# Kernel optimization log

Measured on AMD Instinct MI355X. Metric: run time of the kernel, lower is better.

Reference implementation:

```python
import jax, jax.numpy as jnp
import numpy as np

EPS = 1e-5
H = 8
N_BUCKETS = 32


def _instance_norm(x, gamma, beta):
    # x: [B, N, D]; torch InstanceNorm1d normalizes over the N (length) dim
    # per channel per batch element, using biased variance.
    m = jnp.mean(x, axis=1, keepdims=True)
    v = jnp.var(x, axis=1, keepdims=True)
    return (x - m) * jax.lax.rsqrt(v + EPS) * gamma + beta


def setup_inputs() -> dict:
    key = jax.random.key(0)
    ks = jax.random.split(key, 12)
    B, N, D, d_ff = 4, 512, 128, 512
    s = 1.0 / np.sqrt(D)
    sf = 1.0 / np.sqrt(d_ff)
    u = lambda k, shape, lim: jax.random.uniform(k, shape, jnp.float32, -lim, lim)
    return {
        "h": jax.random.normal(ks[0], (B, N, D), jnp.float32),
        "coords": jax.random.uniform(ks[1], (B, N, 2), jnp.float32),
        "W_Q": u(ks[2], (D, D), s),
        "W_K": u(ks[3], (D, D), s),
        "W_V": u(ks[4], (D, D), s),
        "W_O": u(ks[5], (D, D), s),
        "emb": jax.random.normal(ks[6], (N_BUCKETS, D), jnp.float32),  # n_heads*d_k == D
        "ffn_w1": u(ks[7], (D, d_ff), s),
        "ffn_b1": u(ks[8], (d_ff,), s),
        "ffn_w2": u(ks[9], (d_ff, D), sf),
        "ffn_b2": u(ks[10], (D,), sf),
        "gamma1": jnp.ones((D,), jnp.float32),
        "beta1": jnp.zeros((D,), jnp.float32),
        "gamma2": jnp.ones((D,), jnp.float32),
        "beta2": jnp.zeros((D,), jnp.float32),
    }


def reference(h, coords, W_Q, W_K, W_V, W_O, emb, ffn_w1, ffn_b1, ffn_w2,
              ffn_b2, gamma1, beta1, gamma2, beta2):
    B, N, D = h.shape
    Dk = D // H
    Q = (h @ W_Q).reshape(B, N, H, Dk)
    K = (h @ W_K).reshape(B, N, H, Dk)
    V = (h @ W_V).reshape(B, N, H, Dk)
    # content scores: [B, H, N, N]
    scores = jnp.einsum('bnhd,bmhd->bhnm', Q, K) / np.sqrt(Dk)
    # relative-distance bucket embeddings for all (i, j) pairs
    diff = coords[:, :, None, :] - coords[:, None, :, :]          # [B,N,N,2]
    dist = jax.lax.stop_gradient(jnp.sqrt(jnp.sum(diff * diff, -1)))
    buckets = jnp.clip((dist * N_BUCKETS).astype(jnp.int32), 0, N_BUCKETS - 1)
    r = emb[buckets].reshape(B, N, N, H, Dk)                      # [B,N,N,H,Dk]
    scores = scores + jnp.einsum('bnhd,bnmhd->bhnm', Q, r)
    attn = jax.nn.softmax(scores, axis=-1)
    h_attn = jnp.einsum('bhnm,bmhd->bnhd', attn, V).reshape(B, N, D) @ W_O
    h1 = _instance_norm(h + h_attn, gamma1, beta1)
    h_ffn = jax.nn.relu(h1 @ ffn_w1 + ffn_b1) @ ffn_w2 + ffn_b2
    return _instance_norm(h1 + h_ffn, gamma2, beta2)
```

## Files before the change

kernel.cpp:

```cpp
#include <hip/hip_runtime.h>
#include <hip/hip_bf16.h>

#define B_  4
#define N_  512
#define D_  128
#define H_  8
#define DK  16
#define DFF 512
#define NB  32
#define KS  8

__global__ __launch_bounds__(256) void qkv_qe_kernel(
    const float* __restrict__ A,
    const float* __restrict__ WQ, const float* __restrict__ WK, const float* __restrict__ WV,
    const float* __restrict__ emb,
    float* __restrict__ Qo, float* __restrict__ Ko, float* __restrict__ Vo,
    float* __restrict__ QE)
{
    const float* Bw = blockIdx.z == 0 ? WQ : (blockIdx.z == 1 ? WK : WV);
    float*       C  = blockIdx.z == 0 ? Qo : (blockIdx.z == 1 ? Ko : Vo);
    const int wave = threadIdx.x >> 6;
    const int lane = threadIdx.x & 63;
    const int rbase = __builtin_amdgcn_readfirstlane((blockIdx.x * 4 + wave) * 2);
    const int col = lane * 2;

    float acc[2][2] = {};
#pragma unroll 2
    for (int k0 = 0; k0 < D_; k0 += 4) {
        float4 a0 = *(const float4*)&A[(size_t)(rbase + 0) * D_ + k0];
        float4 a1 = *(const float4*)&A[(size_t)(rbase + 1) * D_ + k0];
#pragma unroll
        for (int kk = 0; kk < 4; ++kk) {
            float2 bv = *(const float2*)&Bw[(size_t)(k0 + kk) * D_ + col];
            float x0 = (&a0.x)[kk], x1 = (&a1.x)[kk];
            acc[0][0] += x0 * bv.x; acc[0][1] += x0 * bv.y;
            acc[1][0] += x1 * bv.x; acc[1][1] += x1 * bv.y;
        }
    }
    *(float2*)&C[(size_t)(rbase + 0) * D_ + col] = make_float2(acc[0][0], acc[0][1]);
    *(float2*)&C[(size_t)(rbase + 1) * D_ + col] = make_float2(acc[1][0], acc[1][1]);

    if (blockIdx.z == 0) {
        __shared__ float Qls[8][132];
        *(float2*)&Qls[wave * 2 + 0][col] = make_float2(acc[0][0], acc[0][1]);
        *(float2*)&Qls[wave * 2 + 1][col] = make_float2(acc[1][0], acc[1][1]);
        __syncthreads();
        const int r  = threadIdx.x >> 5;
        const int hh = (threadIdx.x >> 2) & 7;
        const int k0 = (threadIdx.x & 3) * 8;
        const int grow = blockIdx.x * 8 + r;
        const float4* qv = (const float4*)&Qls[r][hh * DK];
        const float4 qa = qv[0], qb = qv[1], qc = qv[2], qd = qv[3];
        float* qe_out = QE + ((size_t)grow * H_ + hh) * NB + k0;
#pragma unroll 2
        for (int k = 0; k < 8; ++k) {
            const float4* ep = (const float4*)(emb + (size_t)(k0 + k) * D_ + hh * DK);
            float4 e0 = ep[0], e1 = ep[1], e2 = ep[2], e3 = ep[3];
            float d0 = fmaf(qa.x,e0.x, fmaf(qa.y,e0.y, fmaf(qa.z,e0.z, qa.w*e0.w)));
            float d1 = fmaf(qb.x,e1.x, fmaf(qb.y,e1.y, fmaf(qb.z,e1.z, qb.w*e1.w)));
            float d2 = fmaf(qc.x,e2.x, fmaf(qc.y,e2.y, fmaf(qc.z,e2.z, qc.w*e2.w)));
            float d3 = fmaf(qd.x,e3.x, fmaf(qd.y,e3.y, fmaf(qd.z,e3.z, qd.w*e3.w)));
            qe_out[k] = (d0 + d1) + (d2 + d3);
        }
    }
}

__global__ __launch_bounds__(256) void attn6_kernel(
    const float* __restrict__ Q, const float* __restrict__ K, const float* __restrict__ V,
    const float* __restrict__ QE, const float* __restrict__ coords,
    float* __restrict__ P)
{
    const int tid  = threadIdx.x;
    const int wave = tid >> 6;
    const int lane = tid & 63;
    const int bid  = blockIdx.x;
    const int ks    = bid & 7;
    const int chunk = (bid >> 3) & 7;
    const int h     = (bid >> 6) & (H_ - 1);
    const int b     = bid >> 9;
    const int row = b * N_ + chunk * 64 + lane;

    __shared__ float kl[64][16];
    __shared__ float vl[64][16];
    __shared__ float qel[64][NB + 1];
    __shared__ float ckrd[64][2];
    __shared__ float accl[4][64][17];

    const size_t hdbase = (size_t)b * N_ * D_ + h * DK;
    {
        int key = tid >> 2, part = tid & 3;
        size_t g = hdbase + (size_t)(ks * 64 + key) * D_ + part * 4;
        *(float4*)&kl[key][part * 4] = *(const float4*)&K[g];
        *(float4*)&vl[key][part * 4] = *(const float4*)&V[g];
    }
    {
        int r = tid >> 2, part = tid & 3;
        const float* src = QE + ((size_t)(b * N_ + chunk * 64 + r) * H_ + h) * NB + part * 8;
#pragma unroll
        for (int j = 0; j < 8; ++j) qel[r][part * 8 + j] = src[j];
    }
    if (tid < 128)
        ((float*)ckrd)[tid] = coords[(size_t)(b * N_ + ks * 64) * 2 + tid];

    const float4* qp = (const float4*)(Q + (size_t)row * D_ + h * DK);
    const float4 q0 = qp[0], q1 = qp[1], q2 = qp[2], q3 = qp[3];
    const float cx = coords[(size_t)row * 2 + 0];
    const float cy = coords[(size_t)row * 2 + 1];

    __syncthreads();

    float l = 0.f;
    float acc[16] = {};
    const int ml0 = wave * 16;
#pragma unroll 4
    for (int i = 0; i < 16; ++i) {
        const int ml = ml0 + i;
        float dx = cx - ckrd[ml][0], dy = cy - ckrd[ml][1];
        float dist = sqrtf(fmaf(dx, dx, dy * dy));
        int bucket = (int)(dist * 32.0f);
        bucket = bucket > (NB - 1) ? (NB - 1) : bucket;
        float qe = qel[lane][bucket];
        const float4* kp = (const float4*)&kl[ml][0];
        const float4 k0 = kp[0], k1 = kp[1], k2 = kp[2], k3 = kp[3];
        float d0 = fmaf(q0.x,k0.x, fmaf(q0.y,k0.y, fmaf(q0.z,k0.z, q0.w*k0.w)));
        float d1 = fmaf(q1.x,k1.x, fmaf(q1.y,k1.y, fmaf(q1.z,k1.z, q1.w*k1.w)));
        float d2 = fmaf(q2.x,k2.x, fmaf(q2.y,k2.y, fmaf(q2.z,k2.z, q2.w*k2.w)));
        float d3 = fmaf(q3.x,k3.x, fmaf(q3.y,k3.y, fmaf(q3.z,k3.z, q3.w*k3.w)));
        float p = __expf(fmaf((d0 + d1) + (d2 + d3), 0.25f, qe));
        l += p;
        const float4* vp = (const float4*)&vl[ml][0];
        const float4 v0 = vp[0], v1 = vp[1], v2 = vp[2], v3 = vp[3];
        acc[0]  += p * v0.x; acc[1]  += p * v0.y; acc[2]  += p * v0.z; acc[3]  += p * v0.w;
        acc[4]  += p * v1.x; acc[5]  += p * v1.y; acc[6]  += p * v1.z; acc[7]  += p * v1.w;
        acc[8]  += p * v2.x; acc[9]  += p * v2.y; acc[10] += p * v2.z; acc[11] += p * v2.w;
        acc[12] += p * v3.x; acc[13] += p * v3.y; acc[14] += p * v3.z; acc[15] += p * v3.w;
    }

    accl[wave][lane][16] = l;
#pragma unroll
    for (int j = 0; j < 16; ++j) accl[wave][lane][j] = acc[j];
    __syncthreads();

    float* pb = P + (size_t)bid * (64 * 17);
    for (int i = tid; i < 64 * 17; i += 256) {
        int r = i / 17, j = i - r * 17;
        pb[i] = accl[0][r][j] + accl[1][r][j] + accl[2][r][j] + accl[3][r][j];
    }
}

__global__ __launch_bounds__(256) void oproj_kernel(
    const float* __restrict__ P, const float* __restrict__ WO,
    const float* __restrict__ hres, float* __restrict__ X1)
{
    const int tid = threadIdx.x;
    const int gr0 = blockIdx.x * 8;
    __shared__ float AOls[8][128];
    __shared__ float lsl[8][8];

    if (tid < 64) {
        int r = tid >> 3, hh = tid & 7;
        int gr = gr0 + r;
        int b = gr >> 9, n = gr & (N_ - 1);
        int chunk = n >> 6, rl = n & 63;
        size_t base = ((size_t)(((b * H_ + hh) * 8 + chunk) * KS)) * (64 * 17) + (size_t)rl * 17;
        float l = 0.f;
#pragma unroll
        for (int s = 0; s < KS; ++s) l += P[base + (size_t)s * (64 * 17) + 16];
        lsl[r][hh] = l;
    }
    float asum[4];
#pragma unroll
    for (int j = 0; j < 4; ++j) {
        int i = tid + j * 256;
        int r = i >> 7, d = i & 127;
        int gr = gr0 + r;
        int b = gr >> 9, n = gr & (N_ - 1);
        int chunk = n >> 6, rl = n & 63;
        int hh = d >> 4, dk = d & 15;
        size_t base = ((size_t)(((b * H_ + hh) * 8 + chunk) * KS)) * (64 * 17) + (size_t)rl * 17 + dk;
        float s = 0.f;
#pragma unroll
        for (int ss = 0; ss < KS; ++ss) s += P[base + (size_t)ss * (64 * 17)];
        asum[j] = s;
    }
    __syncthreads();
#pragma unroll
    for (int j = 0; j < 4; ++j) {
        int i = tid + j * 256;
        int r = i >> 7, d = i & 127;
        AOls[r][d] = asum[j] / lsl[r][d >> 4];
    }
    __syncthreads();

    const int wave = tid >> 6;
    const int lane = tid & 63;
    const int rl = wave * 2;
    const int grb = __builtin_amdgcn_readfirstlane(gr0 + rl);
    const int col = lane * 2;

    float acc[2][2] = {};
#pragma unroll 2
    for (int k0 = 0; k0 < D_; k0 += 4) {
        float4 a0 = *(const float4*)&AOls[rl + 0][k0];
        float4 a1 = *(const float4*)&AOls[rl + 1][k0];
#pragma unroll
        for (int kk = 0; kk < 4; ++kk) {
            float2 bv = *(const float2*)&WO[(size_t)(k0 + kk) * D_ + col];
            float x0 = (&a0.x)[kk], x1 = (&a1.x)[kk];
            acc[0][0] += x0 * bv.x; acc[0][1] += x0 * bv.y;
            acc[1][0] += x1 * bv.x; acc[1][1] += x1 * bv.y;
        }
    }
#pragma unroll
    for (int j = 0; j < 2; ++j) {
        float2 rv = *(const float2*)&hres[(size_t)(grb + j) * D_ + col];
        *(float2*)&X1[(size_t)(grb + j) * D_ + col] =
            make_float2(acc[j][0] + rv.x, acc[j][1] + rv.y);
    }
}

__global__ __launch_bounds__(256) void stats_kernel(const float* __restrict__ X,
    const float* __restrict__ gamma, const float* __restrict__ beta,
    float* __restrict__ T1, float* __restrict__ T2)
{
    const int b  = blockIdx.x >> 5;
    const int dg = blockIdx.x & 31;
    const int dl = threadIdx.x & 3;
    const int nc = threadIdx.x >> 2;
    const float* xp = X + ((size_t)b * N_ + nc * 8) * D_ + dg * 4 + dl;
    float s = 0.f, q = 0.f;
#pragma unroll
    for (int i = 0; i < 8; ++i) { float x = xp[(size_t)i * D_]; s += x; q += x * x; }
    __shared__ float rs[64][4], rq[64][4];
    rs[nc][dl] = s; rq[nc][dl] = q;
    __syncthreads();
    for (int off = 32; off >= 1; off >>= 1) {
        if (nc < off) { rs[nc][dl] += rs[nc + off][dl]; rq[nc][dl] += rq[nc + off][dl]; }
        __syncthreads();
    }
    if (threadIdx.x < 4) {
        int d = dg * 4 + threadIdx.x;
        float mean = rs[0][threadIdx.x] * (1.0f / N_);
        float var  = rq[0][threadIdx.x] * (1.0f / N_) - mean * mean;
        float r = 1.0f / sqrtf(var + 1e-5f);
        float t1 = r * gamma[d];
        T1[b * D_ + d] = t1;
        T2[b * D_ + d] = beta[d] - mean * t1;
    }
}

__global__ __launch_bounds__(256) void ffn1_kernel(
    const float* __restrict__ X1, const float* __restrict__ T1, const float* __restrict__ T2,
    const float* __restrict__ w1, const float* __restrict__ b1, float* __restrict__ F1)
{
    __shared__ float Als[16][128];
    const int gr0 = blockIdx.x * 16;
    const int b = gr0 >> 9;
#pragma unroll
    for (int i = threadIdx.x * 4; i < 16 * 128; i += 1024) {
        int r = i >> 7, c = i & 127;
        float4 x  = *(const float4*)&X1[(size_t)(gr0 + r) * D_ + c];
        float4 t1 = *(const float4*)&T1[b * D_ + c];
        float4 t2 = *(const float4*)&T2[b * D_ + c];
        float4 y;
        y.x = x.x * t1.x + t2.x; y.y = x.y * t1.y + t2.y;
        y.z = x.z * t1.z + t2.z; y.w = x.w * t1.w + t2.w;
        *(float4*)&Als[r][c] = y;
    }
    __syncthreads();

    const int wave = threadIdx.x >> 6;
    const int lane = threadIdx.x & 63;
    const int rl = wave * 4;
    const int col = blockIdx.y * 128 + lane * 2;

    float acc[4][2] = {};
#pragma unroll 2
    for (int k0 = 0; k0 < D_; k0 += 4) {
        float4 a4[4];
#pragma unroll
        for (int j = 0; j < 4; ++j) a4[j] = *(const float4*)&Als[rl + j][k0];
#pragma unroll
        for (int kk = 0; kk < 4; ++kk) {
            float2 bv = *(const float2*)&w1[(size_t)(k0 + kk) * DFF + col];
#pragma unroll
            for (int j = 0; j < 4; ++j) {
                float x = (&a4[j].x)[kk];
                acc[j][0] += x * bv.x; acc[j][1] += x * bv.y;
            }
        }
    }
    float2 bb = *(const float2*)&b1[col];
#pragma unroll
    for (int j = 0; j < 4; ++j) {
        float o0 = fmaxf(acc[j][0] + bb.x, 0.f);
        float o1 = fmaxf(acc[j][1] + bb.y, 0.f);
        *(float2*)&F1[(size_t)(gr0 + rl + j) * DFF + col] = make_float2(o0, o1);
    }
}

__global__ __launch_bounds__(256) void ffn2f_kernel(
    const float* __restrict__ F1, const float* __restrict__ w2, const float* __restrict__ b2,
    const float* __restrict__ X1, const float* __restrict__ T1, const float* __restrict__ T2,
    float* __restrict__ X2)
{
    const int tid = threadIdx.x;
    const int wave = tid >> 6;
    const int lane = tid & 63;
    const int gr0 = __builtin_amdgcn_readfirstlane(blockIdx.x * 4);
    const int kbeg = __builtin_amdgcn_readfirstlane(wave * 128);
    const int col = lane * 2;

    __shared__ float part[4][4][128];

    float acc[4][2] = {};
#pragma unroll 2
    for (int k0 = kbeg; k0 < kbeg + 128; k0 += 4) {
        float4 a4[4];
#pragma unroll
        for (int j = 0; j < 4; ++j)
            a4[j] = *(const float4*)&F1[(size_t)(gr0 + j) * DFF + k0];
#pragma unroll
        for (int kk = 0; kk < 4; ++kk) {
            float2 bv = *(const float2*)&w2[(size_t)(k0 + kk) * D_ + col];
#pragma unroll
            for (int j = 0; j < 4; ++j) {
                float x = (&a4[j].x)[kk];
                acc[j][0] += x * bv.x; acc[j][1] += x * bv.y;
            }
        }
    }
#pragma unroll
    for (int j = 0; j < 4; ++j)
        *(float2*)&part[wave][j][col] = make_float2(acc[j][0], acc[j][1]);
    __syncthreads();

#pragma unroll
    for (int e = 0; e < 2; ++e) {
        int i = tid + e * 256;
        int r = i >> 7, c = i & 127;
        int row = gr0 + r;
        int b = row >> 9;
        float s = part[0][r][c] + part[1][r][c] + part[2][r][c] + part[3][r][c];
        float x1 = X1[(size_t)row * D_ + c];
        float o = s + b2[c] + (x1 * T1[b * D_ + c] + T2[b * D_ + c]);
        X2[(size_t)row * D_ + c] = o;
    }
}

__global__ __launch_bounds__(256) void stats_apply_kernel(const float* __restrict__ X,
    const float* __restrict__ gamma, const float* __restrict__ beta,
    float* __restrict__ Y)
{
    const int b  = blockIdx.x >> 5;
    const int dg = blockIdx.x & 31;
    const int dl = threadIdx.x & 3;
    const int nc = threadIdx.x >> 2;
    const float* xp = X + ((size_t)b * N_ + nc * 8) * D_ + dg * 4 + dl;
    float s = 0.f, q = 0.f;
#pragma unroll
    for (int i = 0; i < 8; ++i) { float x = xp[(size_t)i * D_]; s += x; q += x * x; }
    __shared__ float rs[64][4], rq[64][4];
    __shared__ float t1l[4], t2l[4];
    rs[nc][dl] = s; rq[nc][dl] = q;
    __syncthreads();
    for (int off = 32; off >= 1; off >>= 1) {
        if (nc < off) { rs[nc][dl] += rs[nc + off][dl]; rq[nc][dl] += rq[nc + off][dl]; }
        __syncthreads();
    }
    if (threadIdx.x < 4) {
        int d = dg * 4 + threadIdx.x;
        float mean = rs[0][threadIdx.x] * (1.0f / N_);
        float var  = rq[0][threadIdx.x] * (1.0f / N_) - mean * mean;
        float r = 1.0f / sqrtf(var + 1e-5f);
        float t1 = r * gamma[d];
        t1l[threadIdx.x] = t1;
        t2l[threadIdx.x] = beta[d] - mean * t1;
    }
    __syncthreads();
    const float t1 = t1l[dl], t2 = t2l[dl];
    float* yp = Y + ((size_t)b * N_ + nc * 8) * D_ + dg * 4 + dl;
#pragma unroll
    for (int i = 0; i < 8; ++i) yp[(size_t)i * D_] = xp[(size_t)i * D_] * t1 + t2;
}

extern "C" void kernel_launch(void* const* d_in, const int* in_sizes, int n_in,
                              void* d_out, int out_size, void* d_ws, size_t ws_size,
                              hipStream_t stream)
{
    const float* h      = (const float*)d_in[0];
    const float* coords = (const float*)d_in[1];
    const float* W_Q    = (const float*)d_in[2];
    const float* W_K    = (const float*)d_in[3];
    const float* W_V    = (const float*)d_in[4];
    const float* W_O    = (const float*)d_in[5];
    const float* emb    = (const float*)d_in[6];
    const float* w1     = (const float*)d_in[7];
    const float* b1     = (const float*)d_in[8];
    const float* w2     = (const float*)d_in[9];
    const float* b2     = (const float*)d_in[10];
    const float* g1     = (const float*)d_in[11];
    const float* be1    = (const float*)d_in[12];
    const float* g2     = (const float*)d_in[13];
    const float* be2    = (const float*)d_in[14];
    float* out = (float*)d_out;

    float* ws = (float*)d_ws;
    const size_t R = (size_t)B_ * N_;
    float* Qb  = ws;
    float* Kb  = Qb + R * D_;
    float* Vb  = Kb + R * D_;
    float* QEb = Vb + R * D_;
    float* X1  = QEb + R * H_ * NB;
    float* F1  = X1 + R * D_;
    float* X2  = F1 + R * DFF;
    float* Pb  = X2 + R * D_;
    float* T1a = Pb + (size_t)2048 * 64 * 17;
    float* T2a = T1a + B_ * D_;

    qkv_qe_kernel<<<dim3(256, 1, 3), 256, 0, stream>>>(
        h, W_Q, W_K, W_V, emb, Qb, Kb, Vb, QEb);
    attn6_kernel<<<dim3(2048), 256, 0, stream>>>(Qb, Kb, Vb, QEb, coords, Pb);
    oproj_kernel<<<dim3((int)R / 8), 256, 0, stream>>>(Pb, W_O, h, X1);
    stats_kernel<<<dim3(B_ * 32), 256, 0, stream>>>(X1, g1, be1, T1a, T2a);
    ffn1_kernel<<<dim3(128, 4), 256, 0, stream>>>(X1, T1a, T2a, w1, b1, F1);
    ffn2f_kernel<<<dim3((int)R / 4), 256, 0, stream>>>(F1, w2, b2, X1, T1a, T2a, X2);
    stats_apply_kernel<<<dim3(B_ * 32), 256, 0, stream>>>(X2, g2, be2, out);
}
```

Baseline: 80.73 us.

## Fuse instance-norm statistics into GEMM epilogues and drop stats kernel

The o-projection and FFN2 kernels now emit per-block partial column sums and sums of squares. ffn1 reduces those partials to compute the first instance-norm scale and shift itself, which removes the separate stats kernel and one full read of X1. The final norm kernel also reads the partials instead of re-summing X2. Separately, the QKV kernel computes four rows per wave instead of two and launches half as many blocks. This adds redundant partial reductions in every ffn1 block and lowers parallelism in the QKV kernel.

```diff
diff --git a/kernel.cpp b/kernel.cpp
--- a/kernel.cpp
+++ b/kernel.cpp
@@ -21,39 +21,45 @@
     float*       C  = blockIdx.z == 0 ? Qo : (blockIdx.z == 1 ? Ko : Vo);
     const int wave = threadIdx.x >> 6;
     const int lane = threadIdx.x & 63;
-    const int rbase = __builtin_amdgcn_readfirstlane((blockIdx.x * 4 + wave) * 2);
+    const int rbase = __builtin_amdgcn_readfirstlane((blockIdx.x * 4 + wave) * 4);
     const int col = lane * 2;
 
-    float acc[2][2] = {};
+    float acc[4][2] = {};
 #pragma unroll 2
     for (int k0 = 0; k0 < D_; k0 += 4) {
-        float4 a0 = *(const float4*)&A[(size_t)(rbase + 0) * D_ + k0];
-        float4 a1 = *(const float4*)&A[(size_t)(rbase + 1) * D_ + k0];
+        float4 a4[4];
+#pragma unroll
+        for (int j = 0; j < 4; ++j)
+            a4[j] = *(const float4*)&A[(size_t)(rbase + j) * D_ + k0];
 #pragma unroll
         for (int kk = 0; kk < 4; ++kk) {
             float2 bv = *(const float2*)&Bw[(size_t)(k0 + kk) * D_ + col];
-            float x0 = (&a0.x)[kk], x1 = (&a1.x)[kk];
-            acc[0][0] += x0 * bv.x; acc[0][1] += x0 * bv.y;
-            acc[1][0] += x1 * bv.x; acc[1][1] += x1 * bv.y;
-        }
-    }
-    *(float2*)&C[(size_t)(rbase + 0) * D_ + col] = make_float2(acc[0][0], acc[0][1]);
-    *(float2*)&C[(size_t)(rbase + 1) * D_ + col] = make_float2(acc[1][0], acc[1][1]);
+#pragma unroll
+            for (int j = 0; j < 4; ++j) {
+                float x = (&a4[j].x)[kk];
+                acc[j][0] += x * bv.x; acc[j][1] += x * bv.y;
+            }
+        }
+    }
+#pragma unroll
+    for (int j = 0; j < 4; ++j)
+        *(float2*)&C[(size_t)(rbase + j) * D_ + col] = make_float2(acc[j][0], acc[j][1]);
 
     if (blockIdx.z == 0) {
-        __shared__ float Qls[8][132];
-        *(float2*)&Qls[wave * 2 + 0][col] = make_float2(acc[0][0], acc[0][1]);
-        *(float2*)&Qls[wave * 2 + 1][col] = make_float2(acc[1][0], acc[1][1]);
+        __shared__ float Qls[16][132];
+#pragma unroll
+        for (int j = 0; j < 4; ++j)
+            *(float2*)&Qls[wave * 4 + j][col] = make_float2(acc[j][0], acc[j][1]);
         __syncthreads();
-        const int r  = threadIdx.x >> 5;
-        const int hh = (threadIdx.x >> 2) & 7;
-        const int k0 = (threadIdx.x & 3) * 8;
-        const int grow = blockIdx.x * 8 + r;
+        const int r  = threadIdx.x >> 4;
+        const int hh = (threadIdx.x & 15) >> 1;
+        const int k0 = (threadIdx.x & 1) * 16;
+        const int grow = blockIdx.x * 16 + r;
         const float4* qv = (const float4*)&Qls[r][hh * DK];
         const float4 qa = qv[0], qb = qv[1], qc = qv[2], qd = qv[3];
         float* qe_out = QE + ((size_t)grow * H_ + hh) * NB + k0;
-#pragma unroll 2
-        for (int k = 0; k < 8; ++k) {
+#pragma unroll 4
+        for (int k = 0; k < 16; ++k) {
             const float4* ep = (const float4*)(emb + (size_t)(k0 + k) * D_ + hh * DK);
             float4 e0 = ep[0], e1 = ep[1], e2 = ep[2], e3 = ep[3];
             float d0 = fmaf(qa.x,e0.x, fmaf(qa.y,e0.y, fmaf(qa.z,e0.z, qa.w*e0.w)));
@@ -150,12 +156,13 @@
 
 __global__ __launch_bounds__(256) void oproj_kernel(
     const float* __restrict__ P, const float* __restrict__ WO,
-    const float* __restrict__ hres, float* __restrict__ X1)
+    const float* __restrict__ hres, float* __restrict__ X1, float* __restrict__ PS1)
 {
     const int tid = threadIdx.x;
     const int gr0 = blockIdx.x * 8;
     __shared__ float AOls[8][128];
     __shared__ float lsl[8][8];
+    __shared__ float psum[4][128], psq[4][128];
 
     if (tid < 64) {
         int r = tid >> 3, hh = tid & 7;
@@ -211,158 +218,190 @@
             acc[1][0] += x1 * bv.x; acc[1][1] += x1 * bv.y;
         }
     }
+    float o[2][2];
 #pragma unroll
     for (int j = 0; j < 2; ++j) {
         float2 rv = *(const float2*)&hres[(size_t)(grb + j) * D_ + col];
-        *(float2*)&X1[(size_t)(grb + j) * D_ + col] =
-            make_float2(acc[j][0] + rv.x, acc[j][1] + rv.y);
-    }
-}
-
-__global__ __launch_bounds__(256) void stats_kernel(const float* __restrict__ X,
+        o[j][0] = acc[j][0] + rv.x;
+        o[j][1] = acc[j][1] + rv.y;
+        *(float2*)&X1[(size_t)(grb + j) * D_ + col] = make_float2(o[j][0], o[j][1]);
+    }
+    psum[wave][col]     = o[0][0] + o[1][0];
+    psum[wave][col + 1] = o[0][1] + o[1][1];
+    psq[wave][col]      = o[0][0]*o[0][0] + o[1][0]*o[1][0];
+    psq[wave][col + 1]  = o[0][1]*o[0][1] + o[1][1]*o[1][1];
+    __syncthreads();
+    if (tid < 128) {
+        float S = (psum[0][tid] + psum[1][tid]) + (psum[2][tid] + psum[3][tid]);
+        float Q = (psq[0][tid]  + psq[1][tid])  + (psq[2][tid]  + psq[3][tid]);
+        PS1[(size_t)blockIdx.x * 256 + tid]       = S;
+        PS1[(size_t)blockIdx.x * 256 + 128 + tid] = Q;
+    }
+}
+
+__global__ __launch_bounds__(256) void ffn1_kernel(
+    const float* __restrict__ X1, const float* __restrict__ PS1,
+    const float* __restrict__ g1, const float* __restrict__ be1,
+    const float* __restrict__ w1, const float* __restrict__ b1,
+    float* __restrict__ F1, float* __restrict__ T1a, float* __restrict__ T2a)
+{
+    const int tid = threadIdx.x;
+    const int gr0 = blockIdx.x * 16;
+    const int b = gr0 >> 9;
+
+    __shared__ float red[2][2][128];
+    __shared__ float t1l[128], t2l[128];
+    __shared__ float Als[16][128];
+
+    {
+        int d = tid & 127, half = tid >> 7;
+        const float* base = PS1 + (size_t)(64 * b + half * 32) * 256;
+        float s0=0,s1=0,s2=0,s3=0, q0=0,q1=0,q2=0,q3=0;
+#pragma unroll
+        for (int j = 0; j < 32; j += 4) {
+            s0 += base[(size_t)(j+0)*256 + d];       q0 += base[(size_t)(j+0)*256 + 128 + d];
+            s1 += base[(size_t)(j+1)*256 + d];       q1 += base[(size_t)(j+1)*256 + 128 + d];
+            s2 += base[(size_t)(j+2)*256 + d];       q2 += base[(size_t)(j+2)*256 + 128 + d];
+            s3 += base[(size_t)(j+3)*256 + d];       q3 += base[(size_t)(j+3)*256 + 128 + d];
+        }
+        red[half][0][d] = (s0 + s1) + (s2 + s3);
+        red[half][1][d] = (q0 + q1) + (q2 + q3);
+    }
+    __syncthreads();
+    if (tid < 128) {
+        float S  = red[0][0][tid] + red[1][0][tid];
+        float Q2 = red[0][1][tid] + red[1][1][tid];
+        float mean = S * (1.0f / N_);
+        float var  = Q2 * (1.0f / N_) - mean * mean;
+        float r = 1.0f / sqrtf(var + 1e-5f);
+        float t1 = r * g1[tid];
+        float t2 = be1[tid] - mean * t1;
+        t1l[tid] = t1; t2l[tid] = t2;
+        if (blockIdx.y == 0) {
+            T1a[b * D_ + tid] = t1;
+            T2a[b * D_ + tid] = t2;
+        }
+    }
+    __syncthreads();
+
+#pragma unroll
+    for (int i = tid * 4; i < 16 * 128; i += 1024) {
+        int r = i >> 7, c = i & 127;
+        float4 x = *(const float4*)&X1[(size_t)(gr0 + r) * D_ + c];
+        float4 y;
+        y.x = x.x * t1l[c+0] + t2l[c+0]; y.y = x.y * t1l[c+1] + t2l[c+1];
+        y.z = x.z * t1l[c+2] + t2l[c+2]; y.w = x.w * t1l[c+3] + t2l[c+3];
+        *(float4*)&Als[r][c] = y;
+    }
+    __syncthreads();
+
+    const int wave = tid >> 6;
+    const int lane = tid & 63;
+    const int rl = wave * 4;
+    const int col = blockIdx.y * 128 + lane * 2;
+
+    float acc[4][2] = {};
+#pragma unroll 2
+    for (int k0 = 0; k0 < D_; k0 += 4) {
+        float4 a4[4];
+#pragma unroll
+        for (int j = 0; j < 4; ++j) a4[j] = *(const float4*)&Als[rl + j][k0];
+#pragma unroll
+        for (int kk = 0; kk < 4; ++kk) {
+            float2 bv = *(const float2*)&w1[(size_t)(k0 + kk) * DFF + col];
+#pragma unroll
+            for (int j = 0; j < 4; ++j) {
+                float x = (&a4[j].x)[kk];
+                acc[j][0] += x * bv.x; acc[j][1] += x * bv.y;
+            }
+        }
+    }
+    float2 bb = *(const float2*)&b1[col];
+#pragma unroll
+    for (int j = 0; j < 4; ++j) {
+        float o0 = fmaxf(acc[j][0] + bb.x, 0.f);
+        float o1 = fmaxf(acc[j][1] + bb.y, 0.f);
+        *(float2*)&F1[(size_t)(gr0 + rl + j) * DFF + col] = make_float2(o0, o1);
+    }
+}
+
+__global__ __launch_bounds__(256) void ffn2f_kernel(
+    const float* __restrict__ F1, const float* __restrict__ w2, const float* __restrict__ b2,
+    const float* __restrict__ X1, const float* __restrict__ T1, const float* __restrict__ T2,
+    float* __restrict__ X2, float* __restrict__ PS2)
+{
+    const int tid = threadIdx.x;
+    const int wave = tid >> 6;
+    const int lane = tid & 63;
+    const int gr0 = __builtin_amdgcn_readfirstlane(blockIdx.x * 4);
+    const int kbeg = wave * 128;
+    const int col = lane * 2;
+
+    __shared__ float part[4][4][128];
+    __shared__ float p2s[2][128], p2q[2][128];
+
+    float acc[4][2] = {};
+#pragma unroll 2
+    for (int k0 = kbeg; k0 < kbeg + 128; k0 += 4) {
+        float4 a4[4];
+#pragma unroll
+        for (int j = 0; j < 4; ++j)
+            a4[j] = *(const float4*)&F1[(size_t)(gr0 + j) * DFF + k0];
+#pragma unroll
+        for (int kk = 0; kk < 4; ++kk) {
+            float2 bv = *(const float2*)&w2[(size_t)(k0 + kk) * D_ + col];
+#pragma unroll
+            for (int j = 0; j < 4; ++j) {
+                float x = (&a4[j].x)[kk];
+                acc[j][0] += x * bv.x; acc[j][1] += x * bv.y;
+            }
+        }
+    }
+#pragma unroll
+    for (int j = 0; j < 4; ++j)
+        *(float2*)&part[wave][j][col] = make_float2(acc[j][0], acc[j][1]);
+    __syncthreads();
+
+    const int c = tid & 127;
+    const int h = tid >> 7;
+    const int bb = gr0 >> 9;
+    float sacc = 0.f, qacc = 0.f;
+#pragma unroll
+    for (int e = 0; e < 2; ++e) {
+        int r = h + e * 2;
+        int row = gr0 + r;
+        float s = part[0][r][c] + part[1][r][c] + part[2][r][c] + part[3][r][c];
+        float x1 = X1[(size_t)row * D_ + c];
+        float o = s + b2[c] + (x1 * T1[bb * D_ + c] + T2[bb * D_ + c]);
+        X2[(size_t)row * D_ + c] = o;
+        sacc += o; qacc += o * o;
+    }
+    p2s[h][c] = sacc; p2q[h][c] = qacc;
+    __syncthreads();
+    if (tid < 128) {
+        PS2[(size_t)blockIdx.x * 256 + tid]       = p2s[0][tid] + p2s[1][tid];
+        PS2[(size_t)blockIdx.x * 256 + 128 + tid] = p2q[0][tid] + p2q[1][tid];
+    }
+}
+
+__global__ __launch_bounds__(256) void stats_apply_kernel(const float* __restrict__ X,
+    const float* __restrict__ PS2,
     const float* __restrict__ gamma, const float* __restrict__ beta,
-    float* __restrict__ T1, float* __restrict__ T2)
+    float* __restrict__ Y)
 {
     const int b  = blockIdx.x >> 5;
     const int dg = blockIdx.x & 31;
     const int dl = threadIdx.x & 3;
     const int nc = threadIdx.x >> 2;
-    const float* xp = X + ((size_t)b * N_ + nc * 8) * D_ + dg * 4 + dl;
-    float s = 0.f, q = 0.f;
-#pragma unroll
-    for (int i = 0; i < 8; ++i) { float x = xp[(size_t)i * D_]; s += x; q += x * x; }
-    __shared__ float rs[64][4], rq[64][4];
-    rs[nc][dl] = s; rq[nc][dl] = q;
-    __syncthreads();
-    for (int off = 32; off >= 1; off >>= 1) {
-        if (nc < off) { rs[nc][dl] += rs[nc + off][dl]; rq[nc][dl] += rq[nc + off][dl]; }
-        __syncthreads();
-    }
-    if (threadIdx.x < 4) {
-        int d = dg * 4 + threadIdx.x;
-        float mean = rs[0][threadIdx.x] * (1.0f / N_);
-        float var  = rq[0][threadIdx.x] * (1.0f / N_) - mean * mean;
-        float r = 1.0f / sqrtf(var + 1e-5f);
-        float t1 = r * gamma[d];
-        T1[b * D_ + d] = t1;
-        T2[b * D_ + d] = beta[d] - mean * t1;
-    }
-}
-
-__global__ __launch_bounds__(256) void ffn1_kernel(
-    const float* __restrict__ X1, const float* __restrict__ T1, const float* __restrict__ T2,
-    const float* __restrict__ w1, const float* __restrict__ b1, float* __restrict__ F1)
-{
-    __shared__ float Als[16][128];
-    const int gr0 = blockIdx.x * 16;
-    const int b = gr0 >> 9;
-#pragma unroll
-    for (int i = threadIdx.x * 4; i < 16 * 128; i += 1024) {
-        int r = i >> 7, c = i & 127;
-        float4 x  = *(const float4*)&X1[(size_t)(gr0 + r) * D_ + c];
-        float4 t1 = *(const float4*)&T1[b * D_ + c];
-        float4 t2 = *(const float4*)&T2[b * D_ + c];
-        float4 y;
-        y.x = x.x * t1.x + t2.x; y.y = x.y * t1.y + t2.y;
-        y.z = x.z * t1.z + t2.z; y.w = x.w * t1.w + t2.w;
-        *(float4*)&Als[r][c] = y;
-    }
-    __syncthreads();
-
-    const int wave = threadIdx.x >> 6;
-    const int lane = threadIdx.x & 63;
-    const int rl = wave * 4;
-    const int col = blockIdx.y * 128 + lane * 2;
-
-    float acc[4][2] = {};
-#pragma unroll 2
-    for (int k0 = 0; k0 < D_; k0 += 4) {
-        float4 a4[4];
-#pragma unroll
-        for (int j = 0; j < 4; ++j) a4[j] = *(const float4*)&Als[rl + j][k0];
-#pragma unroll
-        for (int kk = 0; kk < 4; ++kk) {
-            float2 bv = *(const float2*)&w1[(size_t)(k0 + kk) * DFF + col];
-#pragma unroll
-            for (int j = 0; j < 4; ++j) {
-                float x = (&a4[j].x)[kk];
-                acc[j][0] += x * bv.x; acc[j][1] += x * bv.y;
-            }
-        }
-    }
-    float2 bb = *(const float2*)&b1[col];
-#pragma unroll
-    for (int j = 0; j < 4; ++j) {
-        float o0 = fmaxf(acc[j][0] + bb.x, 0.f);
-        float o1 = fmaxf(acc[j][1] + bb.y, 0.f);
-        *(float2*)&F1[(size_t)(gr0 + rl + j) * DFF + col] = make_float2(o0, o1);
-    }
-}
-
-__global__ __launch_bounds__(256) void ffn2f_kernel(
-    const float* __restrict__ F1, const float* __restrict__ w2, const float* __restrict__ b2,
-    const float* __restrict__ X1, const float* __restrict__ T1, const float* __restrict__ T2,
-    float* __restrict__ X2)
-{
-    const int tid = threadIdx.x;
-    const int wave = tid >> 6;
-    const int lane = tid & 63;
-    const int gr0 = __builtin_amdgcn_readfirstlane(blockIdx.x * 4);
-    const int kbeg = __builtin_amdgcn_readfirstlane(wave * 128);
-    const int col = lane * 2;
-
-    __shared__ float part[4][4][128];
-
-    float acc[4][2] = {};
-#pragma unroll 2
-    for (int k0 = kbeg; k0 < kbeg + 128; k0 += 4) {
-        float4 a4[4];
-#pragma unroll
-        for (int j = 0; j < 4; ++j)
-            a4[j] = *(const float4*)&F1[(size_t)(gr0 + j) * DFF + k0];
-#pragma unroll
-        for (int kk = 0; kk < 4; ++kk) {
-            float2 bv = *(const float2*)&w2[(size_t)(k0 + kk) * D_ + col];
-#pragma unroll
-            for (int j = 0; j < 4; ++j) {
-                float x = (&a4[j].x)[kk];
-                acc[j][0] += x * bv.x; acc[j][1] += x * bv.y;
-            }
-        }
-    }
-#pragma unroll
-    for (int j = 0; j < 4; ++j)
-        *(float2*)&part[wave][j][col] = make_float2(acc[j][0], acc[j][1]);
-    __syncthreads();
-
-#pragma unroll
-    for (int e = 0; e < 2; ++e) {
-        int i = tid + e * 256;
-        int r = i >> 7, c = i & 127;
-        int row = gr0 + r;
-        int b = row >> 9;
-        float s = part[0][r][c] + part[1][r][c] + part[2][r][c] + part[3][r][c];
-        float x1 = X1[(size_t)row * D_ + c];
-        float o = s + b2[c] + (x1 * T1[b * D_ + c] + T2[b * D_ + c]);
-        X2[(size_t)row * D_ + c] = o;
-    }
-}
-
-__global__ __launch_bounds__(256) void stats_apply_kernel(const float* __restrict__ X,
-    const float* __restrict__ gamma, const float* __restrict__ beta,
-    float* __restrict__ Y)
-{
-    const int b  = blockIdx.x >> 5;
-    const int dg = blockIdx.x & 31;
-    const int dl = threadIdx.x & 3;
-    const int nc = threadIdx.x >> 2;
-    const float* xp = X + ((size_t)b * N_ + nc * 8) * D_ + dg * 4 + dl;
-    float s = 0.f, q = 0.f;
-#pragma unroll
-    for (int i = 0; i < 8; ++i) { float x = xp[(size_t)i * D_]; s += x; q += x * x; }
     __shared__ float rs[64][4], rq[64][4];
     __shared__ float t1l[4], t2l[4];
-    rs[nc][dl] = s; rq[nc][dl] = q;
+
+    {
+        const float* pbase = PS2 + (size_t)(128 * b + nc * 2) * 256;
+        int d = dg * 4 + dl;
+        rs[nc][dl] = pbase[d] + pbase[256 + d];
+        rq[nc][dl] = pbase[128 + d] + pbase[256 + 128 + d];
+    }
     __syncthreads();
     for (int off = 32; off >= 1; off >>= 1) {
         if (nc < off) { rs[nc][dl] += rs[nc + off][dl]; rq[nc][dl] += rq[nc + off][dl]; }
@@ -379,6 +418,7 @@
     }
     __syncthreads();
     const float t1 = t1l[dl], t2 = t2l[dl];
+    const float* xp = X + ((size_t)b * N_ + nc * 8) * D_ + dg * 4 + dl;
     float* yp = Y + ((size_t)b * N_ + nc * 8) * D_ + dg * 4 + dl;
 #pragma unroll
     for (int i = 0; i < 8; ++i) yp[(size_t)i * D_] = xp[(size_t)i * D_] * t1 + t2;
@@ -415,15 +455,16 @@
     float* F1  = X1 + R * D_;
     float* X2  = F1 + R * DFF;
     float* Pb  = X2 + R * D_;
-    float* T1a = Pb + (size_t)2048 * 64 * 17;
+    float* PS1 = Pb + (size_t)2048 * 64 * 17;
+    float* PS2 = PS1 + 256 * 256;
+    float* T1a = PS2 + 512 * 256;
     float* T2a = T1a + B_ * D_;
 
-    qkv_qe_kernel<<<dim3(256, 1, 3), 256, 0, stream>>>(
+    qkv_qe_kernel<<<dim3(128, 1, 3), 256, 0, stream>>>(
         h, W_Q, W_K, W_V, emb, Qb, Kb, Vb, QEb);
     attn6_kernel<<<dim3(2048), 256, 0, stream>>>(Qb, Kb, Vb, QEb, coords, Pb);
-    oproj_kernel<<<dim3((int)R / 8), 256, 0, stream>>>(Pb, W_O, h, X1);
-    stats_kernel<<<dim3(B_ * 32), 256, 0, stream>>>(X1, g1, be1, T1a, T2a);
-    ffn1_kernel<<<dim3(128, 4), 256, 0, stream>>>(X1, T1a, T2a, w1, b1, F1);
-    ffn2f_kernel<<<dim3((int)R / 4), 256, 0, stream>>>(F1, w2, b2, X1, T1a, T2a, X2);
-    stats_apply_kernel<<<dim3(B_ * 32), 256, 0, stream>>>(X2, g2, be2, out);
-}
+    oproj_kernel<<<dim3((int)R / 8), 256, 0, stream>>>(Pb, W_O, h, X1, PS1);
+    ffn1_kernel<<<dim3(128, 4), 256, 0, stream>>>(X1, PS1, g1, be1, w1, b1, F1, T1a, T2a);
+    ffn2f_kernel<<<dim3((int)R / 4), 256, 0, stream>>>(F1, w2, b2, X1, T1a, T2a, X2, PS2);
+    stats_apply_kernel<<<dim3(B_ * 32), 256, 0, stream>>>(X2, PS2, g2, be2, out);
+}
```

Result: slower. 84.13 us (+4.2%).
